# Optimization experiments

Measured on AMD Instinct MI355X. Metric: run time of the kernel, lower is better.

Reference implementation:

```python
import jax, jax.numpy as jnp
import numpy as np

POOL_VOLUME = 8  # prod(pool_size) = 2*2*2 for dimension=3

N_IN = 1500000
N_OUT = 375000
C = 64

def setup_inputs() -> dict:
    key = jax.random.key(0)
    k1, k2, k3 = jax.random.split(key, 3)
    input_features = jax.random.normal(k1, (N_IN, C), dtype=jnp.float32)
    # Rulebook: (input_row, output_row) pairs; with pool=stride=2 each active
    # input site contributes to exactly one output site.
    rules_in = jax.random.randint(k2, (N_IN,), 0, N_IN, dtype=jnp.int32)
    rules_out = jax.random.randint(k3, (N_IN,), 0, N_OUT, dtype=jnp.int32)
    return {
        "input_features": input_features,
        "rules_in": rules_in,
        "rules_out": rules_out,
        "n_out": N_OUT,
    }

def reference(input_features, rules_in, rules_out, n_out):
    # Sparse average pooling: gather active input rows per rulebook entry,
    # segment-sum into output sites, normalize by the fixed filter volume
    # (SCN AveragePooling divides by prod(pool_size), not active count).
    gathered = input_features[rules_in] * (1.0 / POOL_VOLUME)  # [n_rules, C]
    out = jax.ops.segment_sum(gathered, rules_out, num_segments=n_out)  # [n_out, C]
    return out
```

## Files before the change

kernel.cpp:

```cpp
#include <hip/hip_runtime.h>


#define C_CHANNELS 64
#define ROW_INTS 16
#define CAP_ENT 15
#define OVF_CAP 16384

typedef float f32x4 __attribute__((ext_vector_type(4)));

__global__ __launch_bounds__(256) void
zero_ws_kernel(int4* __restrict__ p, int n4, int* __restrict__ ovf_cnt) {
    int i = blockIdx.x * blockDim.x + threadIdx.x;
    int stride = gridDim.x * blockDim.x;
    int4 z = make_int4(0, 0, 0, 0);
    for (; i < n4; i += stride) p[i] = z;
    if (blockIdx.x == 0 && threadIdx.x == 0) *ovf_cnt = 0;
}

__device__ __forceinline__ void
push_rule(int ri, int ro,
          int* __restrict__ bucket,
          int* __restrict__ ovf_cnt,
          int2* __restrict__ ovf_pairs) {
    int* row = bucket + (size_t)ro * ROW_INTS;
    int pos = atomicAdd(row, 1);
    if (pos < CAP_ENT) {
        row[1 + pos] = ri;
    } else {
        int oi = atomicAdd(ovf_cnt, 1);
        if (oi < OVF_CAP) ovf_pairs[oi] = make_int2(ri, ro);
    }
}

__global__ __launch_bounds__(256) void
build_kernel(const int* __restrict__ rules_in,
             const int* __restrict__ rules_out,
             int* __restrict__ bucket,
             int* __restrict__ ovf_cnt,
             int2* __restrict__ ovf_pairs,
             int n_rules) {
    int t = blockIdx.x * blockDim.x + threadIdx.x;
    int r0 = t << 2;
    if (r0 >= n_rules) return;
    if (r0 + 4 <= n_rules) {
        int4 ri4 = *reinterpret_cast<const int4*>(rules_in + r0);
        int4 ro4 = *reinterpret_cast<const int4*>(rules_out + r0);
        push_rule(ri4.x, ro4.x, bucket, ovf_cnt, ovf_pairs);
        push_rule(ri4.y, ro4.y, bucket, ovf_cnt, ovf_pairs);
        push_rule(ri4.z, ro4.z, bucket, ovf_cnt, ovf_pairs);
        push_rule(ri4.w, ro4.w, bucket, ovf_cnt, ovf_pairs);
    } else {
        for (int r = r0; r < n_rules; ++r)
            push_rule(rules_in[r], rules_out[r], bucket, ovf_cnt, ovf_pairs);
    }
}

__global__ __launch_bounds__(256) void
gather_kernel(const float* __restrict__ in,
              const int* __restrict__ bucket,
              float* __restrict__ out,
              int n_out) {
    int idx = blockIdx.x * blockDim.x + threadIdx.x;
    int ro = idx >> 4;
    int c4 = (idx & 15) << 2;
    if (ro >= n_out) return;

    const int4* row = reinterpret_cast<const int4*>(bucket + (size_t)ro * ROW_INTS);
    int4 q0 = row[0];
    int4 q1 = row[1];
    int k = q0.x < CAP_ENT ? q0.x : CAP_ENT;

    f32x4 s = {0.f, 0.f, 0.f, 0.f};

#define ACC(ridx) \
    s += *reinterpret_cast<const f32x4*>(in + (size_t)(unsigned)(ridx) * C_CHANNELS + c4)

    if (k > 0) {
        ACC(q0.y);
        if (k > 1)  ACC(q0.z);
        if (k > 2)  ACC(q0.w);
        if (k > 3)  ACC(q1.x);
        if (k > 4)  ACC(q1.y);
        if (k > 5)  ACC(q1.z);
        if (k > 6)  ACC(q1.w);
        if (k > 7) {
            int4 q2 = row[2];
            ACC(q2.x);
            if (k > 8)  ACC(q2.y);
            if (k > 9)  ACC(q2.z);
            if (k > 10) ACC(q2.w);
            if (k > 11) {
                int4 q3 = row[3];
                ACC(q3.x);
                if (k > 12) ACC(q3.y);
                if (k > 13) ACC(q3.z);
                if (k > 14) ACC(q3.w);
            }
        }
    }
#undef ACC

    f32x4 o = s * 0.125f;
    __builtin_nontemporal_store(
        o, reinterpret_cast<f32x4*>(out + (size_t)ro * C_CHANNELS + c4));
}

__global__ __launch_bounds__(256) void
ovf_scatter_kernel(const float* __restrict__ in,
                   const int* __restrict__ ovf_cnt,
                   const int2* __restrict__ ovf_pairs,
                   float* __restrict__ out) {
    int n = *ovf_cnt;
    if (n > OVF_CAP) n = OVF_CAP;
    int total = n * 16;
    int stride = gridDim.x * blockDim.x;
    for (int idx = blockIdx.x * blockDim.x + threadIdx.x; idx < total; idx += stride) {
        int p  = idx >> 4;
        int c4 = (idx & 15) << 2;
        int2 pr = ovf_pairs[p];
        const float4 v = *reinterpret_cast<const float4*>(
            in + (size_t)pr.x * C_CHANNELS + c4);
        float* o = out + (size_t)pr.y * C_CHANNELS + c4;
        atomicAdd(o + 0, v.x * 0.125f);
        atomicAdd(o + 1, v.y * 0.125f);
        atomicAdd(o + 2, v.z * 0.125f);
        atomicAdd(o + 3, v.w * 0.125f);
    }
}

__global__ __launch_bounds__(256) void
zero4_kernel(float4* __restrict__ p, long n4) {
    long i = (long)blockIdx.x * blockDim.x + threadIdx.x;
    long stride = (long)gridDim.x * blockDim.x;
    float4 z = {0.f, 0.f, 0.f, 0.f};
    for (; i < n4; i += stride) p[i] = z;
}

__global__ __launch_bounds__(256) void
avgpool_scatter_kernel(const float* __restrict__ in,
                       const int* __restrict__ rules_in,
                       const int* __restrict__ rules_out,
                       float* __restrict__ out,
                       int n_rules) {
    int idx = blockIdx.x * blockDim.x + threadIdx.x;
    int rule = idx >> 4;
    int c4   = (idx & 15) << 2;
    if (rule >= n_rules) return;
    int ri = rules_in[rule];
    int ro = rules_out[rule];
    const float4 v = *reinterpret_cast<const float4*>(
        in + (size_t)ri * C_CHANNELS + c4);
    float* o = out + (size_t)ro * C_CHANNELS + c4;
    atomicAdd(o + 0, v.x * 0.125f);
    atomicAdd(o + 1, v.y * 0.125f);
    atomicAdd(o + 2, v.z * 0.125f);
    atomicAdd(o + 3, v.w * 0.125f);
}

extern "C" void kernel_launch(void* const* d_in, const int* in_sizes, int n_in,
                              void* d_out, int out_size, void* d_ws, size_t ws_size,
                              hipStream_t stream) {
    const float* in        = (const float*)d_in[0];
    const int*   rules_in  = (const int*)d_in[1];
    const int*   rules_out = (const int*)d_in[2];
    float*       out       = (float*)d_out;

    const int n_rules = in_sizes[1];
    const int n_out   = out_size / C_CHANNELS;

    size_t list_bytes = (size_t)n_out * ROW_INTS * sizeof(int);
    size_t list_pad   = (list_bytes + 15) & ~(size_t)15;
    size_t ovf_hdr    = 16;
    size_t need = list_pad + ovf_hdr + (size_t)OVF_CAP * sizeof(int2);

    const int block = 256;

    if (ws_size < need) {
        long n4 = (long)out_size / 4;
        int grid = (int)((n4 + block - 1) / block);
        if (grid > 65535) grid = 65535;
        zero4_kernel<<<grid, block, 0, stream>>>((float4*)out, n4);
        int total = n_rules * 16;
        avgpool_scatter_kernel<<<(total + block - 1) / block, block, 0, stream>>>(
            in, rules_in, rules_out, out, n_rules);
        return;
    }

    int*  bucket    = (int*)d_ws;
    int*  ovf_cnt   = (int*)((char*)d_ws + list_pad);
    int2* ovf_pairs = (int2*)((char*)d_ws + list_pad + ovf_hdr);

    {
        int n4 = (int)(list_bytes / 16);
        int grid = (n4 + block - 1) / block;
        zero_ws_kernel<<<grid, block, 0, stream>>>((int4*)bucket, n4, ovf_cnt);
    }

    {
        int threads = (n_rules + 3) / 4;
        build_kernel<<<(threads + block - 1) / block, block, 0, stream>>>(
            rules_in, rules_out, bucket, ovf_cnt, ovf_pairs, n_rules);
    }

    {
        long total = (long)n_out * 16;
        int grid = (int)((total + block - 1) / block);
        gather_kernel<<<grid, block, 0, stream>>>(in, bucket, out, n_out);
    }

    ovf_scatter_kernel<<<64, block, 0, stream>>>(in, ovf_cnt, ovf_pairs, out);
}
```

Measured before the change: 602.7 us.

## Process two output rows per thread with speculative branchless gathers

The gather kernel now has each thread handle two output rows, one from each half of the output. It loads the first seven indexed input rows for both outputs unconditionally and masks unused slots with a multiply by zero instead of branching, which raises the number of loads in flight to hide gather latency. Unused bucket slots are zero, so the masked loads read input row 0; that is wasted bandwidth, and a non-finite value in row 0 would turn into NaN. Bucket metadata is read with nontemporal loads, and the build kernel now takes two rules per thread and issues both atomics before either store.

```diff
diff --git a/kernel.cpp b/kernel.cpp
--- a/kernel.cpp
+++ b/kernel.cpp
@@ -7,6 +7,7 @@
 #define OVF_CAP 16384
 
 typedef float f32x4 __attribute__((ext_vector_type(4)));
+typedef int   i32x4 __attribute__((ext_vector_type(4)));
 
 __global__ __launch_bounds__(256) void
 zero_ws_kernel(int4* __restrict__ p, int n4, int* __restrict__ ovf_cnt) {
@@ -18,12 +19,8 @@
 }
 
 __device__ __forceinline__ void
-push_rule(int ri, int ro,
-          int* __restrict__ bucket,
-          int* __restrict__ ovf_cnt,
-          int2* __restrict__ ovf_pairs) {
-    int* row = bucket + (size_t)ro * ROW_INTS;
-    int pos = atomicAdd(row, 1);
+store_entry(int* __restrict__ row, int pos, int ri,
+            int ro, int* __restrict__ ovf_cnt, int2* __restrict__ ovf_pairs) {
     if (pos < CAP_ENT) {
         row[1 + pos] = ri;
     } else {
@@ -40,18 +37,22 @@
              int2* __restrict__ ovf_pairs,
              int n_rules) {
     int t = blockIdx.x * blockDim.x + threadIdx.x;
-    int r0 = t << 2;
+    int r0 = t << 1;
     if (r0 >= n_rules) return;
-    if (r0 + 4 <= n_rules) {
-        int4 ri4 = *reinterpret_cast<const int4*>(rules_in + r0);
-        int4 ro4 = *reinterpret_cast<const int4*>(rules_out + r0);
-        push_rule(ri4.x, ro4.x, bucket, ovf_cnt, ovf_pairs);
-        push_rule(ri4.y, ro4.y, bucket, ovf_cnt, ovf_pairs);
-        push_rule(ri4.z, ro4.z, bucket, ovf_cnt, ovf_pairs);
-        push_rule(ri4.w, ro4.w, bucket, ovf_cnt, ovf_pairs);
+    if (r0 + 2 <= n_rules) {
+        int2 ri2 = *reinterpret_cast<const int2*>(rules_in + r0);
+        int2 ro2 = *reinterpret_cast<const int2*>(rules_out + r0);
+        int* pa = bucket + (size_t)ro2.x * ROW_INTS;
+        int* pb = bucket + (size_t)ro2.y * ROW_INTS;
+        int sa = atomicAdd(pa, 1);
+        int sb = atomicAdd(pb, 1);
+        store_entry(pa, sa, ri2.x, ro2.x, ovf_cnt, ovf_pairs);
+        store_entry(pb, sb, ri2.y, ro2.y, ovf_cnt, ovf_pairs);
     } else {
-        for (int r = r0; r < n_rules; ++r)
-            push_rule(rules_in[r], rules_out[r], bucket, ovf_cnt, ovf_pairs);
+        int ro = rules_out[r0];
+        int* row = bucket + (size_t)ro * ROW_INTS;
+        int pos = atomicAdd(row, 1);
+        store_entry(row, pos, rules_in[r0], ro, ovf_cnt, ovf_pairs);
     }
 }
 
@@ -61,48 +62,109 @@
               float* __restrict__ out,
               int n_out) {
     int idx = blockIdx.x * blockDim.x + threadIdx.x;
-    int ro = idx >> 4;
+    int pair = idx >> 4;
     int c4 = (idx & 15) << 2;
-    if (ro >= n_out) return;
-
-    const int4* row = reinterpret_cast<const int4*>(bucket + (size_t)ro * ROW_INTS);
-    int4 q0 = row[0];
-    int4 q1 = row[1];
-    int k = q0.x < CAP_ENT ? q0.x : CAP_ENT;
-
-    f32x4 s = {0.f, 0.f, 0.f, 0.f};
-
-#define ACC(ridx) \
-    s += *reinterpret_cast<const f32x4*>(in + (size_t)(unsigned)(ridx) * C_CHANNELS + c4)
-
-    if (k > 0) {
-        ACC(q0.y);
-        if (k > 1)  ACC(q0.z);
-        if (k > 2)  ACC(q0.w);
-        if (k > 3)  ACC(q1.x);
-        if (k > 4)  ACC(q1.y);
-        if (k > 5)  ACC(q1.z);
-        if (k > 6)  ACC(q1.w);
-        if (k > 7) {
-            int4 q2 = row[2];
-            ACC(q2.x);
-            if (k > 8)  ACC(q2.y);
-            if (k > 9)  ACC(q2.z);
-            if (k > 10) ACC(q2.w);
-            if (k > 11) {
-                int4 q3 = row[3];
-                ACC(q3.x);
-                if (k > 12) ACC(q3.y);
-                if (k > 13) ACC(q3.z);
-                if (k > 14) ACC(q3.w);
-            }
-        }
-    }
-#undef ACC
-
-    f32x4 o = s * 0.125f;
+    int half = (n_out + 1) >> 1;
+    if (pair >= half) return;
+
+    int roA = pair;
+    int roB = pair + half;
+    bool hasB = roB < n_out;
+    int roBs = hasB ? roB : roA;
+
+    const i32x4* rowA = reinterpret_cast<const i32x4*>(bucket + (size_t)roA * ROW_INTS);
+    const i32x4* rowB = reinterpret_cast<const i32x4*>(bucket + (size_t)roBs * ROW_INTS);
+    i32x4 a0 = __builtin_nontemporal_load(&rowA[0]);
+    i32x4 a1 = __builtin_nontemporal_load(&rowA[1]);
+    i32x4 b0 = __builtin_nontemporal_load(&rowB[0]);
+    i32x4 b1 = __builtin_nontemporal_load(&rowB[1]);
+    int kA = a0.x < CAP_ENT ? a0.x : CAP_ENT;
+    int kB = b0.x < CAP_ENT ? b0.x : CAP_ENT;
+
+    const float* base = in + c4;
+#define LDV(r) (*reinterpret_cast<const f32x4*>(base + (size_t)(unsigned)(r) * C_CHANNELS))
+
+    f32x4 va0 = LDV(a0.y);
+    f32x4 va1 = LDV(a0.z);
+    f32x4 va2 = LDV(a0.w);
+    f32x4 va3 = LDV(a1.x);
+    f32x4 va4 = LDV(a1.y);
+    f32x4 va5 = LDV(a1.z);
+    f32x4 va6 = LDV(a1.w);
+    f32x4 vb0 = LDV(b0.y);
+    f32x4 vb1 = LDV(b0.z);
+    f32x4 vb2 = LDV(b0.w);
+    f32x4 vb3 = LDV(b1.x);
+    f32x4 vb4 = LDV(b1.y);
+    f32x4 vb5 = LDV(b1.z);
+    f32x4 vb6 = LDV(b1.w);
+
+    f32x4 sA = va0 * (kA > 0 ? 1.f : 0.f);
+    sA += va1 * (kA > 1 ? 1.f : 0.f);
+    sA += va2 * (kA > 2 ? 1.f : 0.f);
+    sA += va3 * (kA > 3 ? 1.f : 0.f);
+    sA += va4 * (kA > 4 ? 1.f : 0.f);
+    sA += va5 * (kA > 5 ? 1.f : 0.f);
+    sA += va6 * (kA > 6 ? 1.f : 0.f);
+
+    f32x4 sB = vb0 * (kB > 0 ? 1.f : 0.f);
+    sB += vb1 * (kB > 1 ? 1.f : 0.f);
+    sB += vb2 * (kB > 2 ? 1.f : 0.f);
+    sB += vb3 * (kB > 3 ? 1.f : 0.f);
+    sB += vb4 * (kB > 4 ? 1.f : 0.f);
+    sB += vb5 * (kB > 5 ? 1.f : 0.f);
+    sB += vb6 * (kB > 6 ? 1.f : 0.f);
+
+    if (kA > 7) {
+        i32x4 a2 = __builtin_nontemporal_load(&rowA[2]);
+        i32x4 a3 = __builtin_nontemporal_load(&rowA[3]);
+        f32x4 w0 = LDV(a2.x);
+        f32x4 w1 = LDV(a2.y);
+        f32x4 w2 = LDV(a2.z);
+        f32x4 w3 = LDV(a2.w);
+        f32x4 w4 = LDV(a3.x);
+        f32x4 w5 = LDV(a3.y);
+        f32x4 w6 = LDV(a3.z);
+        f32x4 w7 = LDV(a3.w);
+        sA += w0;
+        sA += w1 * (kA > 8  ? 1.f : 0.f);
+        sA += w2 * (kA > 9  ? 1.f : 0.f);
+        sA += w3 * (kA > 10 ? 1.f : 0.f);
+        sA += w4 * (kA > 11 ? 1.f : 0.f);
+        sA += w5 * (kA > 12 ? 1.f : 0.f);
+        sA += w6 * (kA > 13 ? 1.f : 0.f);
+        sA += w7 * (kA > 14 ? 1.f : 0.f);
+    }
+    if (kB > 7) {
+        i32x4 b2 = __builtin_nontemporal_load(&rowB[2]);
+        i32x4 b3 = __builtin_nontemporal_load(&rowB[3]);
+        f32x4 w0 = LDV(b2.x);
+        f32x4 w1 = LDV(b2.y);
+        f32x4 w2 = LDV(b2.z);
+        f32x4 w3 = LDV(b2.w);
+        f32x4 w4 = LDV(b3.x);
+        f32x4 w5 = LDV(b3.y);
+        f32x4 w6 = LDV(b3.z);
+        f32x4 w7 = LDV(b3.w);
+        sB += w0;
+        sB += w1 * (kB > 8  ? 1.f : 0.f);
+        sB += w2 * (kB > 9  ? 1.f : 0.f);
+        sB += w3 * (kB > 10 ? 1.f : 0.f);
+        sB += w4 * (kB > 11 ? 1.f : 0.f);
+        sB += w5 * (kB > 12 ? 1.f : 0.f);
+        sB += w6 * (kB > 13 ? 1.f : 0.f);
+        sB += w7 * (kB > 14 ? 1.f : 0.f);
+    }
+#undef LDV
+
+    f32x4 oA = sA * 0.125f;
     __builtin_nontemporal_store(
-        o, reinterpret_cast<f32x4*>(out + (size_t)ro * C_CHANNELS + c4));
+        oA, reinterpret_cast<f32x4*>(out + (size_t)roA * C_CHANNELS + c4));
+    if (hasB) {
+        f32x4 oB = sB * 0.125f;
+        __builtin_nontemporal_store(
+            oB, reinterpret_cast<f32x4*>(out + (size_t)roB * C_CHANNELS + c4));
+    }
 }
 
 __global__ __launch_bounds__(256) void
@@ -197,13 +259,14 @@
     }
 
     {
-        int threads = (n_rules + 3) / 4;
+        int threads = (n_rules + 1) / 2;
         build_kernel<<<(threads + block - 1) / block, block, 0, stream>>>(
             rules_in, rules_out, bucket, ovf_cnt, ovf_pairs, n_rules);
     }
 
     {
-        long total = (long)n_out * 16;
+        long half = (n_out + 1) >> 1;
+        long total = half * 16;
         int grid = (int)((total + block - 1) / block);
         gather_kernel<<<grid, block, 0, stream>>>(in, bucket, out, n_out);
     }
```

Result: no change. 600.1 us (-0.4%).
